# Optimization experiments

Hardware: AMD Instinct MI355X
Metric: run time of the kernel (lower is better)

The kernel has to match this reference:

```python
import jax, jax.numpy as jnp
import numpy as np
from jax import lax

D, H, DK, L, FF, V, B, S = 384, 12, 32, 6, 1536, 30522, 16, 512

def _logit(p):
    return float(np.log(p / (1.0 - p)))

def setup_inputs():
    key = jax.random.key(0)
    ks = jax.random.split(key, 16)
    def g(i, shape, scale=0.02):
        return jax.random.normal(ks[i], shape, jnp.float32) * scale
    return {
        "input_ids": jax.random.randint(ks[0], (B, S), 0, V),
        "attention_mask": jnp.ones((B, S), jnp.int32),
        "emb_tok": g(1, (V, D)),
        "emb_pos": g(2, (S, D)),
        "emb_type": g(3, (2, D)),
        "emb_ln_g": jnp.ones((D,), jnp.float32),
        "emb_ln_b": jnp.zeros((D,), jnp.float32),
        "Wq": g(4, (L, D, D)), "bq": jnp.zeros((L, D), jnp.float32),
        "Wk": g(5, (L, D, D)), "bk": jnp.zeros((L, D), jnp.float32),
        "Wv": g(6, (L, D, D)), "bv": jnp.zeros((L, D), jnp.float32),
        "Wbeta": g(7, (L, D, H)), "bbeta": jnp.zeros((L, H), jnp.float32),
        "decay_fast": jnp.full((L, H), _logit(0.3), jnp.float32),
        "decay_slow": jnp.full((L, H), _logit(0.85), jnp.float32),
        "mix_logit": jnp.zeros((L, H), jnp.float32),
        "Wg": g(8, (L, D, D)),
        "Wo": g(9, (L, D, D)), "bo": jnp.zeros((L, D), jnp.float32),
        "attn_ln_g": jnp.ones((L, D), jnp.float32), "attn_ln_b": jnp.zeros((L, D), jnp.float32),
        "Wffn1": g(10, (L, D, FF)), "bffn1": jnp.zeros((L, FF), jnp.float32),
        "Wffn2": g(11, (L, FF, D)), "bffn2": jnp.zeros((L, D), jnp.float32),
        "ffn_ln_g": jnp.ones((L, D), jnp.float32), "ffn_ln_b": jnp.zeros((L, D), jnp.float32),
    }

def _ln(x, g, b, eps=1e-12):
    m = x.mean(-1, keepdims=True)
    v = ((x - m) ** 2).mean(-1, keepdims=True)
    return (x - m) * lax.rsqrt(v + eps) * g + b

def _delta_attn(x, mask_f, Wq, bq, Wk, bk, Wv, bv, Wbeta, bbeta, df_logit, ds_logit, mix_logit, Wg, Wo, bo):
    # Hierarchical delta-rule linear attention: O(n) recurrence, two decay timescales.
    Bz, Sq, _ = x.shape
    q = jax.nn.silu((x @ Wq + bq).reshape(Bz, Sq, H, DK))
    k = jax.nn.silu((x @ Wk + bk).reshape(Bz, Sq, H, DK))
    k = k / (jnp.linalg.norm(k, axis=-1, keepdims=True) + 1e-6)
    v = (x @ Wv + bv).reshape(Bz, Sq, H, DK)
    beta = jax.nn.sigmoid(x @ Wbeta + bbeta) * mask_f[..., None]  # [B,S,H]
    df = jax.nn.sigmoid(df_logit)[None, :, None, None]  # fast decay, per head
    ds = jax.nn.sigmoid(ds_logit)[None, :, None, None]  # slow decay, per head
    qT = q.transpose(1, 0, 2, 3)  # time-major [S,B,H,DK]
    kT = k.transpose(1, 0, 2, 3)
    vT = v.transpose(1, 0, 2, 3)
    betaT = beta.transpose(1, 0, 2)

    def step(carry, xs):
        Sf, Ss = carry  # [B,H,DK,DK] fast/slow memory states
        kt, vt, qt, bt = xs
        err_f = (vt - jnp.einsum('bhk,bhkv->bhv', kt, Sf)) * bt[..., None]
        Sf = df * Sf + jnp.einsum('bhk,bhv->bhkv', kt, err_f)
        err_s = (vt - jnp.einsum('bhk,bhkv->bhv', kt, Ss)) * bt[..., None]
        Ss = ds * Ss + jnp.einsum('bhk,bhv->bhkv', kt, err_s)
        of = jnp.einsum('bhk,bhkv->bhv', qt, Sf)
        os = jnp.einsum('bhk,bhkv->bhv', qt, Ss)
        return (Sf, Ss), (of, os)

    S0 = jnp.zeros((Bz, H, DK, DK), x.dtype)
    _, (ofT, osT) = lax.scan(step, (S0, S0), (kT, vT, qT, betaT))
    mix = jax.nn.sigmoid(mix_logit)[None, None, :, None]
    o = mix * ofT.transpose(1, 0, 2, 3) + (1.0 - mix) * osT.transpose(1, 0, 2, 3)
    o = o.reshape(Bz, Sq, D)
    o = o * jax.nn.sigmoid(x @ Wg)  # enhanced-flux output gate
    return o @ Wo + bo

def reference(input_ids, attention_mask, emb_tok, emb_pos, emb_type, emb_ln_g, emb_ln_b, Wq, bq, Wk, bk, Wv, bv, Wbeta, bbeta, decay_fast, decay_slow, mix_logit, Wg, Wo, bo, attn_ln_g, attn_ln_b, Wffn1, bffn1, Wffn2, bffn2, ffn_ln_g, ffn_ln_b):
    mask_f = attention_mask.astype(jnp.float32)
    h = emb_tok[input_ids] + emb_pos[None, :input_ids.shape[1]] + emb_type[0][None, None]
    h = _ln(h, emb_ln_g, emb_ln_b)
    for i in range(L):
        attn = _delta_attn(h, mask_f, Wq[i], bq[i], Wk[i], bk[i], Wv[i], bv[i], Wbeta[i], bbeta[i], decay_fast[i], decay_slow[i], mix_logit[i], Wg[i], Wo[i], bo[i])
        h = _ln(h + attn, attn_ln_g[i], attn_ln_b[i])
        ffn = jax.nn.gelu(h @ Wffn1[i] + bffn1[i], approximate=False) @ Wffn2[i] + bffn2[i]
        h = _ln(h + ffn, ffn_ln_g[i], ffn_ln_b[i])
    m = mask_f[..., None]
    emb = (h * m).sum(1) / jnp.clip(m.sum(1), 1e-9)
    return emb / (jnp.linalg.norm(emb, axis=1, keepdims=True) + 1e-12)
```

## Files before the change

kernel.cpp:

```cpp
#include <hip/hip_runtime.h>
#include <hip/hip_bf16.h>

#define NTOK   8192
#define DMODEL 384
#define NHEAD  12
#define DHEAD  32
#define NLAYER 6
#define DFF    1536
#define SEQ    512
#define BATCH  16
#define WTAL   1916928L

typedef __attribute__((ext_vector_type(8))) short short8;
typedef __attribute__((ext_vector_type(4))) float f32x4;

__device__ __forceinline__ float sigmoidf_(float x){ return 1.f/(1.f+expf(-x)); }

__device__ __forceinline__ ushort f2b(float x){
  uint b = __builtin_bit_cast(uint, x);
  uint r = (b + 0x7FFFu + ((b>>16)&1u)) >> 16;
  return (ushort)r;
}
__device__ __forceinline__ uint pk2(float lo, float hi){
  return (uint)f2b(lo) | ((uint)f2b(hi)<<16);
}
__device__ __forceinline__ float4 b2f4(uint2 u){
  float4 f;
  f.x = __builtin_bit_cast(float, u.x<<16);
  f.y = __builtin_bit_cast(float, u.x & 0xffff0000u);
  f.z = __builtin_bit_cast(float, u.y<<16);
  f.w = __builtin_bit_cast(float, u.y & 0xffff0000u);
  return f;
}
__device__ __forceinline__ float red8(float x){
  int t = __builtin_amdgcn_update_dpp(0, __builtin_bit_cast(int,x), 0xB1, 0xF, 0xF, true);
  x += __builtin_bit_cast(float,t);
  t = __builtin_amdgcn_update_dpp(0, __builtin_bit_cast(int,x), 0x4E, 0xF, 0xF, true);
  x += __builtin_bit_cast(float,t);
  t = __builtin_amdgcn_update_dpp(0, __builtin_bit_cast(int,x), 0x141, 0xF, 0xF, true);
  x += __builtin_bit_cast(float,t);
  return x;
}
__device__ __forceinline__ void gload16(const ushort* g, ushort* l){
  __builtin_amdgcn_global_load_lds((const __attribute__((address_space(1))) void*)g,
                                   (__attribute__((address_space(3))) void*)l, 16, 0, 0);
}

__device__ __forceinline__ void beta_from_row(
    int n, int tid, const float y0, const float y1, const float y2,
    const float* __restrict__ Wb, const float* __restrict__ bbv,
    const int* __restrict__ amask, float* __restrict__ Bb,
    float (*bred)[13])
{
  float part[12];
  #pragma unroll
  for (int hh=0;hh<12;hh++) part[hh]=0.f;
  #pragma unroll
  for (int j=0;j<3;j++){
    int d = tid + j*128;
    float yv = (j==0)?y0:(j==1)?y1:y2;
    const float* wrow = Wb + (long)d*12;
    #pragma unroll
    for (int hh=0;hh<12;hh++) part[hh] += yv * wrow[hh];
  }
  #pragma unroll
  for (int hh=0;hh<12;hh++) bred[tid][hh] = part[hh];
  __syncthreads();
  if (tid < 96){
    int hh = tid>>3, i = tid&7;
    float s = 0.f;
    #pragma unroll
    for (int k=0;k<16;k++) s += bred[i + 8*k][hh];
    s += __shfl_xor(s,1); s += __shfl_xor(s,2); s += __shfl_xor(s,4);
    if (i==0) Bb[(long)n*NHEAD+hh] = (float)amask[n] * sigmoidf_(s + bbv[hh]);
  }
}

__global__ __launch_bounds__(128) void embed_ln_kernel(
    const int* __restrict__ ids, const float* __restrict__ tok,
    const float* __restrict__ pos, const float* __restrict__ typ,
    const float* __restrict__ g, const float* __restrict__ bvec,
    float* __restrict__ out, ushort* __restrict__ outb,
    const float* __restrict__ Wb0, const float* __restrict__ bb0,
    const int* __restrict__ amask, float* __restrict__ Bb)
{
  __shared__ float r1[2], r2[2];
  __shared__ float bred[128][13];
  int n = blockIdx.x;
  int t = n & (SEQ-1);
  int id = ids[n];
  int tid = threadIdx.x;
  float v[3]; float s1=0.f, s2=0.f;
  #pragma unroll
  for (int j=0;j<3;j++){
    int d = tid + j*128;
    float x = tok[(long)id*DMODEL + d] + pos[t*DMODEL + d] + typ[d];
    v[j]=x; s1+=x; s2+=x*x;
  }
  #pragma unroll
  for (int m=1;m<64;m<<=1){ s1 += __shfl_xor(s1,m); s2 += __shfl_xor(s2,m); }
  if ((tid&63)==0){ r1[tid>>6]=s1; r2[tid>>6]=s2; }
  __syncthreads();
  s1 = r1[0]+r1[1]; s2 = r2[0]+r2[1];
  float mean = s1*(1.f/DMODEL);
  float var  = s2*(1.f/DMODEL) - mean*mean;
  float inv  = rsqrtf(var + 1e-12f);
  float y[3];
  #pragma unroll
  for (int j=0;j<3;j++){
    int d = tid + j*128;
    y[j] = (v[j]-mean)*inv*g[d] + bvec[d];
    out[(long)n*DMODEL + d] = y[j];
    outb[(long)n*DMODEL + d] = f2b(y[j]);
  }
  __syncthreads();
  beta_from_row(n, tid, y[0], y[1], y[2], Wb0, bb0, amask, Bb, bred);
}

__global__ __launch_bounds__(128) void add_ln_kernel(
    float* __restrict__ h, const float* __restrict__ res,
    const float* __restrict__ g, const float* __restrict__ bvec,
    ushort* __restrict__ hb,
    const float* __restrict__ Wbn, const float* __restrict__ bbn,
    const int* __restrict__ amask, float* __restrict__ Bb)
{
  __shared__ float r1[2], r2[2];
  __shared__ float bred[128][13];
  int n = blockIdx.x;
  int tid = threadIdx.x;
  float v[3]; float s1=0.f, s2=0.f;
  #pragma unroll
  for (int j=0;j<3;j++){
    int d = tid + j*128;
    float x = h[(long)n*DMODEL + d] + res[(long)n*DMODEL + d];
    v[j]=x; s1+=x; s2+=x*x;
  }
  #pragma unroll
  for (int m=1;m<64;m<<=1){ s1 += __shfl_xor(s1,m); s2 += __shfl_xor(s2,m); }
  if ((tid&63)==0){ r1[tid>>6]=s1; r2[tid>>6]=s2; }
  __syncthreads();
  s1 = r1[0]+r1[1]; s2 = r2[0]+r2[1];
  float mean = s1*(1.f/DMODEL);
  float var  = s2*(1.f/DMODEL) - mean*mean;
  float inv  = rsqrtf(var + 1e-12f);
  float y[3];
  #pragma unroll
  for (int j=0;j<3;j++){
    int d = tid + j*128;
    y[j] = (v[j]-mean)*inv*g[d] + bvec[d];
    h[(long)n*DMODEL + d] = y[j];
    hb[(long)n*DMODEL + d] = f2b(y[j]);
  }
  if (Wbn){
    __syncthreads();
    beta_from_row(n, tid, y[0], y[1], y[2], Wbn, bbn, amask, Bb, bred);
  }
}

__global__ __launch_bounds__(256) void tcvt6(
    const float* __restrict__ Wq, const float* __restrict__ Wk,
    const float* __restrict__ Wv, const float* __restrict__ Wg,
    const float* __restrict__ Wo, const float* __restrict__ W1,
    const float* __restrict__ W2, ushort* __restrict__ WTA)
{
  __shared__ float tile[32][33];
  int l = blockIdx.x / 1872;
  int bid = blockIdx.x % 1872;
  const float* Wq_l = Wq + (long)l*DMODEL*DMODEL;
  const float* Wk_l = Wk + (long)l*DMODEL*DMODEL;
  const float* Wv_l = Wv + (long)l*DMODEL*DMODEL;
  const float* Wg_l = Wg + (long)l*DMODEL*DMODEL;
  const float* Wo_l = Wo + (long)l*DMODEL*DMODEL;
  const float* W1_l = W1 + (long)l*DMODEL*DFF;
  const float* W2_l = W2 + (long)l*DFF*DMODEL;
  ushort* WTAl = WTA + (long)l*WTAL;

  const float* src; long dstbase; int rowlen, Nd, tk, tn, row0;
  if (bid < 720){
    int seg = bid/144, t = bid%144;
    tk = t%12; tn = t/12;
    src = (seg==0)?Wq_l:(seg==1)?Wk_l:(seg==2)?Wv_l:(seg==3)?Wg_l:Wo_l;
    Nd = 384; rowlen = 384;
    if (seg<4){ dstbase=0; row0=seg*384; }
    else      { dstbase=589824; row0=0; }
  } else if (bid < 1296){
    int t = bid-720; tk=t%12; tn=t/12;
    src=W1_l; Nd=DFF; dstbase=737280; row0=0; rowlen=384;
  } else {
    int t = bid-1296; tk=t%48; tn=t/48;
    src=W2_l; Nd=384; dstbase=1327104; row0=0; rowlen=DFF;
  }
  int k0=tk*32, n0=tn*32;
  int tt=threadIdx.x;
  int r=tt>>3, c4=(tt&7)<<2;
  const float* sp = src + (long)(k0+r)*Nd + n0 + c4;
  float4 f = *(const float4*)sp;
  tile[r][c4+0]=f.x; tile[r][c4+1]=f.y; tile[r][c4+2]=f.z; tile[r][c4+3]=f.w;
  __syncthreads();
  ushort4 o;
  o.x=f2b(tile[c4+0][r]); o.y=f2b(tile[c4+1][r]);
  o.z=f2b(tile[c4+2][r]); o.w=f2b(tile[c4+3][r]);
  *(ushort4*)(WTAl + dstbase + (long)(row0+n0+r)*rowlen + k0 + c4) = o;
}

__device__ __forceinline__ int2 xcd_swz(){
  int lin = blockIdx.y*64 + blockIdx.x;
  int nb = gridDim.x*gridDim.y;
  int s = (lin & 7)*(nb>>3) + (lin>>3);
  return make_int2(s & 63, s >> 6);
}

template<int ACT, int OUTBF>
__global__ __launch_bounds__(256) void gemm_bf(
    const ushort* __restrict__ Xb, const ushort* __restrict__ WT,
    const float* __restrict__ bias, void* __restrict__ Cv, int Kd, int Nd)
{
  __shared__ ushort A_lds[128*32];
  __shared__ ushort B_lds[128*32];
  int tid = threadIdx.x;
  int2 bxy = xcd_swz();
  int bm = bxy.x*128, bn = bxy.y*128;
  int w = tid>>6, lane = tid&63;
  int wm = w>>1, wn = w&1;
  f32x4 acc[4][4];
  #pragma unroll
  for (int i=0;i<4;i++)
    #pragma unroll
    for (int j=0;j<4;j++) acc[i][j]=(f32x4)(0.f);

  int cl = lane&15, koff = (lane>>4)*8;
  int srow = w*32 + (lane>>2);
  int scol = (lane&3)*8;
  const ushort* gA0 = Xb + (long)(bm+srow)*Kd + scol;
  const ushort* gA1 = gA0 + 16*(long)Kd;
  const ushort* gB0 = WT + (long)(bn+srow)*Kd + scol;
  const ushort* gB1 = gB0 + 16*(long)Kd;
  ushort* lA = A_lds + w*1024;
  ushort* lB = B_lds + w*1024;

  for (int k0=0; k0<Kd; k0+=32){
    gload16(gA0+k0, lA);
    gload16(gA1+k0, lA+512);
    gload16(gB0+k0, lB);
    gload16(gB1+k0, lB+512);
    __syncthreads();
    short8 bf[4];
    #pragma unroll
    for (int ni=0;ni<4;ni++)
      bf[ni] = *(const short8*)&B_lds[(wn*64+ni*16+cl)*32 + koff];
    #pragma unroll
    for (int mi=0;mi<4;mi++){
      short8 af = *(const short8*)&A_lds[(wm*64+mi*16+cl)*32 + koff];
      #pragma unroll
      for (int ni=0;ni<4;ni++)
        acc[mi][ni] = __builtin_amdgcn_mfma_f32_16x16x32_bf16(af, bf[ni], acc[mi][ni], 0,0,0);
    }
    __syncthreads();
  }

  int rb = (lane>>4)*4;
  #pragma unroll
  for (int ni=0; ni<4; ni++){
    int col = bn + wn*64 + ni*16 + cl;
    float bsv = bias ? bias[col] : 0.f;
    #pragma unroll
    for (int mi=0; mi<4; mi++){
      #pragma unroll
      for (int j=0;j<4;j++){
        int row = bm + wm*64 + mi*16 + rb + j;
        float c = acc[mi][ni][j] + bsv;
        if (ACT==1)      c = c*sigmoidf_(c);
        else if (ACT==2) c = 0.5f*c*(1.f+erff(c*0.70710678118f));
        else if (ACT==3) c = sigmoidf_(c);
        if (OUTBF) ((ushort*)Cv)[(long)row*Nd + col] = f2b(c);
        else       ((float*)Cv)[(long)row*Nd + col] = c;
      }
    }
  }
}

template<int ACT, int OUTBF>
__global__ __launch_bounds__(256) void gemm_bf2(
    const ushort* __restrict__ Xb, const ushort* __restrict__ WT,
    const float* __restrict__ bias, void* __restrict__ Cv, int Kd, int Nd)
{
  __shared__ ushort A_lds[128*32];
  __shared__ ushort B_lds[64*32];
  int tid = threadIdx.x;
  int2 bxy = xcd_swz();
  int bm = bxy.x*128, bn = bxy.y*64;
  int w = tid>>6, lane = tid&63;
  int wm = w>>1, wn = w&1;
  f32x4 acc[4][2];
  #pragma unroll
  for (int i=0;i<4;i++){ acc[i][0]=(f32x4)(0.f); acc[i][1]=(f32x4)(0.f); }

  int cl = lane&15, koff = (lane>>4)*8;
  int srowA = w*32 + (lane>>2);
  int scol = (lane&3)*8;
  const ushort* gA0 = Xb + (long)(bm+srowA)*Kd + scol;
  const ushort* gA1 = gA0 + 16*(long)Kd;
  int srowB = w*16 + (lane>>2);
  const ushort* gB = WT + (long)(bn+srowB)*Kd + scol;
  ushort* lA = A_lds + w*1024;
  ushort* lB = B_lds + w*512;

  for (int k0=0; k0<Kd; k0+=32){
    gload16(gA0+k0, lA);
    gload16(gA1+k0, lA+512);
    gload16(gB+k0, lB);
    __syncthreads();
    short8 b0 = *(const short8*)&B_lds[(wn*32+cl)*32 + koff];
    short8 b1 = *(const short8*)&B_lds[(wn*32+16+cl)*32 + koff];
    #pragma unroll
    for (int mi=0;mi<4;mi++){
      short8 af = *(const short8*)&A_lds[(wm*64+mi*16+cl)*32 + koff];
      acc[mi][0] = __builtin_amdgcn_mfma_f32_16x16x32_bf16(af, b0, acc[mi][0], 0,0,0);
      acc[mi][1] = __builtin_amdgcn_mfma_f32_16x16x32_bf16(af, b1, acc[mi][1], 0,0,0);
    }
    __syncthreads();
  }

  int rb = (lane>>4)*4;
  #pragma unroll
  for (int ni=0; ni<2; ni++){
    int col = bn + wn*32 + ni*16 + cl;
    float bsv = bias ? bias[col] : 0.f;
    #pragma unroll
    for (int mi=0; mi<4; mi++){
      #pragma unroll
      for (int j=0;j<4;j++){
        int row = bm + wm*64 + mi*16 + rb + j;
        float c = acc[mi][ni][j] + bsv;
        if (ACT==1)      c = c*sigmoidf_(c);
        else if (ACT==2) c = 0.5f*c*(1.f+erff(c*0.70710678118f));
        else if (ACT==3) c = sigmoidf_(c);
        if (OUTBF) ((ushort*)Cv)[(long)row*Nd + col] = f2b(c);
        else       ((float*)Cv)[(long)row*Nd + col] = c;
      }
    }
  }
}

__global__ __launch_bounds__(256) void gemm_qkvg(
    const ushort* __restrict__ Xb, const ushort* __restrict__ WT,
    const float* __restrict__ bq, const float* __restrict__ bk,
    const float* __restrict__ bv, ushort* __restrict__ C)
{
  __shared__ ushort A_lds[128*32];
  __shared__ ushort B_lds[128*32];
  int tid = threadIdx.x;
  int2 bxy = xcd_swz();
  int bm = bxy.x*128, bn = bxy.y*128;
  int w = tid>>6, lane = tid&63;
  int wm = w>>1, wn = w&1;
  f32x4 acc[4][4];
  #pragma unroll
  for (int i=0;i<4;i++)
    #pragma unroll
    for (int j=0;j<4;j++) acc[i][j]=(f32x4)(0.f);

  int cl = lane&15, koff = (lane>>4)*8;
  int srow = w*32 + (lane>>2);
  int scol = (lane&3)*8;
  const ushort* gA0 = Xb + (long)(bm+srow)*DMODEL + scol;
  const ushort* gA1 = gA0 + 16*DMODEL;
  const ushort* gB0 = WT + (long)(bn+srow)*DMODEL + scol;
  const ushort* gB1 = gB0 + 16*DMODEL;
  ushort* lA = A_lds + w*1024;
  ushort* lB = B_lds + w*1024;

  for (int k0=0; k0<DMODEL; k0+=32){
    gload16(gA0+k0, lA);
    gload16(gA1+k0, lA+512);
    gload16(gB0+k0, lB);
    gload16(gB1+k0, lB+512);
    __syncthreads();
    short8 bf[4];
    #pragma unroll
    for (int ni=0;ni<4;ni++)
      bf[ni] = *(const short8*)&B_lds[(wn*64+ni*16+cl)*32 + koff];
    #pragma unroll
    for (int mi=0;mi<4;mi++){
      short8 af = *(const short8*)&A_lds[(wm*64+mi*16+cl)*32 + koff];
      #pragma unroll
      for (int ni=0;ni<4;ni++)
        acc[mi][ni] = __builtin_amdgcn_mfma_f32_16x16x32_bf16(af, bf[ni], acc[mi][ni], 0,0,0);
    }
    __syncthreads();
  }

  int seg = bxy.y/3;
  const float* bp = (seg==0)?bq:(seg==1)?bk:(seg==2)?bv:nullptr;
  int boff = seg*384;
  int rb = (lane>>4)*4;
  #pragma unroll
  for (int ni=0; ni<4; ni++){
    int col = bn + wn*64 + ni*16 + cl;
    float bsv = bp ? bp[col-boff] : 0.f;
    #pragma unroll
    for (int mi=0; mi<4; mi++){
      #pragma unroll
      for (int j=0;j<4;j++){
        int row = bm + wm*64 + mi*16 + rb + j;
        float c = acc[mi][ni][j] + bsv;
        if (seg<2)       c = c*sigmoidf_(c);
        else if (seg==3) c = sigmoidf_(c);
        C[(long)row*DFF + col] = f2b(c);
      }
    }
  }
}

__global__ __launch_bounds__(512,2) void scan12_kernel(
    const ushort* __restrict__ QKVGb, const float* __restrict__ Bb,
    const float* __restrict__ dfl, const float* __restrict__ dsl,
    const float* __restrict__ mixl, ushort* __restrict__ OA)
{
  __shared__ float Qc[66][36], Kc[66][36], Vt[32][68], Bc[68], Ofs[2][64][36];
  int bh = blockIdx.x;
  int b = bh / NHEAD, hh = bh - b*NHEAD;
  int tid = threadIdx.x;
  int w = tid>>6, lane = tid&63;
  int st = w>>2, vq = w&3;
  int kq = lane&7, v = vq*8 + (lane>>3);
  float dec = sigmoidf_(st ? dsl[hh] : dfl[hh]);
  float mix = sigmoidf_(mixl[hh]);
  long rowbase = (long)b*SEQ;
  const ushort* rp = QKVGb + rowbase*DFF + hh*32;
  const float* bp = Bb + rowbase*NHEAD + hh;

  int r0 = tid>>3, c40 = (tid&7)<<2;
  float S[4] = {0.f,0.f,0.f,0.f};

  float4 sq, sk, sv; float sb = 0.f;
  {
    long g = (long)r0*DFF;
    sq = b2f4(*(const uint2*)(rp + g + c40));
    sk = b2f4(*(const uint2*)(rp + g + 384 + c40));
    sv = b2f4(*(const uint2*)(rp + g + 768 + c40));
    if (tid < 64) sb = bp[(long)tid*NHEAD];
    float ss = red8(sk.x*sk.x + sk.y*sk.y + sk.z*sk.z + sk.w*sk.w);
    float inv = 1.f/(sqrtf(ss)+1e-6f);
    sk.x*=inv; sk.y*=inv; sk.z*=inv; sk.w*=inv;
    *(float4*)&Qc[r0][c40] = sq;
    *(float4*)&Kc[r0][c40] = sk;
    Vt[c40+0][r0]=sv.x; Vt[c40+1][r0]=sv.y; Vt[c40+2][r0]=sv.z; Vt[c40+3][r0]=sv.w;
    if (tid < 64) Bc[tid] = sb;
  }
  __syncthreads();

  for (int c=0; c<8; ++c){
    if (c < 7){
      long g = (long)((c+1)*64 + r0)*DFF;
      sq = b2f4(*(const uint2*)(rp + g + c40));
      sk = b2f4(*(const uint2*)(rp + g + 384 + c40));
      sv = b2f4(*(const uint2*)(rp + g + 768 + c40));
      if (tid < 64) sb = bp[(long)((c+1)*64 + tid)*NHEAD];
    }
    float4 g4 = b2f4(*(const uint2*)(rp + (long)(c*64 + r0)*DFF + 1152 + c40));
    __builtin_amdgcn_sched_barrier(0);

    float4 kA = *(const float4*)&Kc[0][kq*4];
    float4 qA = *(const float4*)&Qc[0][kq*4];
    float4 kB = *(const float4*)&Kc[1][kq*4];
    float4 qB = *(const float4*)&Qc[1][kq*4];
    float vrA[4], brA[4], vrB[4], brB[4];
    *(float4*)vrA = *(const float4*)&Vt[v][0];
    *(float4*)brA = *(const float4*)&Bc[0];

    for (int t8=0; t8<8; ++t8){
      *(float4*)vrB = *(const float4*)&Vt[v][(2*t8+1)*4];
      *(float4*)brB = *(const float4*)&Bc[(2*t8+1)*4];
      #pragma unroll
      for (int i=0;i<4;i++){
        int t = t8*8 + i;
        float4 kN = *(const float4*)&Kc[t+2][kq*4];
        float4 qN = *(const float4*)&Qc[t+2][kq*4];
        float pa = kA.x*S[0] + kA.y*S[1];
        float pb = kA.z*S[2] + kA.w*S[3];
        float p = red8(pa+pb);
        float err = (vrA[i] - p)*brA[i];
        S[0] = dec*S[0] + kA.x*err;
        S[1] = dec*S[1] + kA.y*err;
        S[2] = dec*S[2] + kA.z*err;
        S[3] = dec*S[3] + kA.w*err;
        float oa = qA.x*S[0] + qA.y*S[1];
        float ob = qA.z*S[2] + qA.w*S[3];
        float o = red8(oa+ob);
        if (kq==0) Ofs[st][t][v] = o;
        kA=kB; qA=qB; kB=kN; qB=qN;
      }
      *(float4*)vrA = *(const float4*)&Vt[v][(2*t8+2)*4];
      *(float4*)brA = *(const float4*)&Bc[(2*t8+2)*4];
      #pragma unroll
      for (int i=0;i<4;i++){
        int t = t8*8 + 4 + i;
        float4 kN = *(const float4*)&Kc[t+2][kq*4];
        float4 qN = *(const float4*)&Qc[t+2][kq*4];
        float pa = kA.x*S[0] + kA.y*S[1];
        float pb = kA.z*S[2] + kA.w*S[3];
        float p = red8(pa+pb);
        float err = (vrB[i] - p)*brB[i];
        S[0] = dec*S[0] + kA.x*err;
        S[1] = dec*S[1] + kA.y*err;
        S[2] = dec*S[2] + kA.z*err;
        S[3] = dec*S[3] + kA.w*err;
        float oa = qA.x*S[0] + qA.y*S[1];
        float ob = qA.z*S[2] + qA.w*S[3];
        float o = red8(oa+ob);
        if (kq==0) Ofs[st][t][v] = o;
        kA=kB; qA=qB; kB=kN; qB=qN;
      }
    }
    __syncthreads();

    {
      float4 of = *(const float4*)&Ofs[0][r0][c40];
      float4 os = *(const float4*)&Ofs[1][r0][c40];
      float a0 = (mix*of.x + (1.f-mix)*os.x)*g4.x;
      float a1 = (mix*of.y + (1.f-mix)*os.y)*g4.y;
      float a2 = (mix*of.z + (1.f-mix)*os.z)*g4.z;
      float a3 = (mix*of.w + (1.f-mix)*os.w)*g4.w;
      uint2 o2; o2.x = pk2(a0,a1); o2.y = pk2(a2,a3);
      *(uint2*)(OA + (rowbase + c*64 + r0)*DMODEL + hh*32 + c40) = o2;
    }
    if (c < 7){
      *(float4*)&Qc[r0][c40] = sq;
      *(float4*)&Kc[r0][c40] = sk;
      Vt[c40+0][r0]=sv.x; Vt[c40+1][r0]=sv.y; Vt[c40+2][r0]=sv.z; Vt[c40+3][r0]=sv.w;
      if (tid < 64) Bc[tid] = sb;
    }
    __syncthreads();
  }
}

__global__ __launch_bounds__(384) void pool_norm_kernel(
    const float* __restrict__ h, const int* __restrict__ mask, float* __restrict__ out)
{
  int b = blockIdx.x; int d = threadIdx.x;
  float s=0.f, ms=0.f;
  for (int t=0;t<SEQ;t++){
    float m = (float)mask[b*SEQ+t];
    s += h[((long)b*SEQ+t)*DMODEL + d]*m;
    ms += m;
  }
  float emb = s / fmaxf(ms, 1e-9f);
  float ss = emb*emb;
  #pragma unroll
  for (int m2=1;m2<64;m2<<=1) ss += __shfl_xor(ss,m2);
  __shared__ float r[6];
  if ((d&63)==0) r[d>>6]=ss;
  __syncthreads();
  ss = r[0]+r[1]+r[2]+r[3]+r[4]+r[5];
  out[b*DMODEL+d] = emb / (sqrtf(ss)+1e-12f);
}

extern "C" void kernel_launch(void* const* d_in, const int* in_sizes, int n_in,
                              void* d_out, int out_size, void* d_ws, size_t ws_size,
                              hipStream_t stream)
{
  const int*   ids   = (const int*)d_in[0];
  const int*   amask = (const int*)d_in[1];
  const float* etok  = (const float*)d_in[2];
  const float* epos  = (const float*)d_in[3];
  const float* etyp  = (const float*)d_in[4];
  const float* elng  = (const float*)d_in[5];
  const float* elnb  = (const float*)d_in[6];
  const float* Wq = (const float*)d_in[7];  const float* bq = (const float*)d_in[8];
  const float* Wk = (const float*)d_in[9];  const float* bk = (const float*)d_in[10];
  const float* Wv = (const float*)d_in[11]; const float* bv = (const float*)d_in[12];
  const float* Wb = (const float*)d_in[13]; const float* bb = (const float*)d_in[14];
  const float* dfl = (const float*)d_in[15];
  const float* dsl = (const float*)d_in[16];
  const float* mixl= (const float*)d_in[17];
  const float* Wg = (const float*)d_in[18];
  const float* Wo = (const float*)d_in[19]; const float* bo = (const float*)d_in[20];
  const float* alng = (const float*)d_in[21]; const float* alnb = (const float*)d_in[22];
  const float* W1 = (const float*)d_in[23]; const float* b1 = (const float*)d_in[24];
  const float* W2 = (const float*)d_in[25]; const float* b2 = (const float*)d_in[26];
  const float* flng = (const float*)d_in[27]; const float* flnb = (const float*)d_in[28];

  float* ws = (float*)d_ws;
  const long TD = (long)NTOK*DMODEL;
  float* h      = ws;
  ushort* hbf   = (ushort*)(h + TD);
  ushort* QKVGb = (ushort*)(h + TD + TD/2);
  ushort* OA    = (ushort*)(h + TD + TD/2 + 2*TD);
  float* Rb     = h + TD + TD/2 + 2*TD + TD/2;
  float* Bb     = Rb + TD;
  ushort* WTA   = (ushort*)(Bb + (long)NTOK*NHEAD);
  ushort* F1B   = QKVGb;

  embed_ln_kernel<<<NTOK,128,0,stream>>>(ids, etok, epos, etyp, elng, elnb, h, hbf,
                                         Wb, bb, amask, Bb);
  tcvt6<<<6*1872,256,0,stream>>>(Wq, Wk, Wv, Wg, Wo, W1, W2, WTA);

  for (int l=0;l<NLAYER;l++){
    ushort* WTAl = WTA + (long)l*WTAL;
    gemm_qkvg<<<dim3(64,12),256,0,stream>>>(hbf, WTAl, bq+l*DMODEL, bk+l*DMODEL, bv+l*DMODEL, QKVGb);
    scan12_kernel<<<BATCH*NHEAD,512,0,stream>>>(QKVGb, Bb, dfl + l*NHEAD, dsl + l*NHEAD, mixl + l*NHEAD, OA);
    gemm_bf2<0,0><<<dim3(64,6),256,0,stream>>>(OA, WTAl+589824, bo + l*DMODEL, Rb, DMODEL, DMODEL);
    add_ln_kernel<<<NTOK,128,0,stream>>>(h, Rb, alng + (long)l*DMODEL, alnb + (long)l*DMODEL, hbf,
                                         nullptr, nullptr, amask, Bb);
    gemm_bf<2,1><<<dim3(64,12),256,0,stream>>>(hbf, WTAl+737280, b1 + (long)l*DFF, F1B, DMODEL, DFF);
    gemm_bf2<0,0><<<dim3(64,6),256,0,stream>>>(F1B, WTAl+1327104, b2 + (long)l*DMODEL, Rb, DFF, DMODEL);
    const float* Wbn = (l+1<NLAYER) ? (Wb + (long)(l+1)*DMODEL*NHEAD) : nullptr;
    const float* bbn = (l+1<NLAYER) ? (bb + (long)(l+1)*NHEAD) : nullptr;
    add_ln_kernel<<<NTOK,128,0,stream>>>(h, Rb, flng + (long)l*DMODEL, flnb + (long)l*DMODEL, hbf,
                                         Wbn, bbn, amask, Bb);
  }

  pool_norm_kernel<<<BATCH,384,0,stream>>>(h, amask, (float*)d_out);
}
```

Before: 1.146 ms.

## Double-buffer LDS tiles in bf16 GEMM kernels to overlap loads with MFMA

Converts the three MFMA GEMM kernels from single-buffered LDS staging, with two barriers per K step, to ping-pong A/B buffers. The next K tile's global-to-LDS load is issued before the current tile's MFMAs, with a single waitcnt and barrier per step. This hides global load latency behind compute and halves barrier count. LDS use doubles per block, which may lower occupancy. The loop also assumes an even number of K iterations.

```diff
diff --git a/kernel.cpp b/kernel.cpp
--- a/kernel.cpp
+++ b/kernel.cpp
@@ -215,8 +215,7 @@
     const ushort* __restrict__ Xb, const ushort* __restrict__ WT,
     const float* __restrict__ bias, void* __restrict__ Cv, int Kd, int Nd)
 {
-  __shared__ ushort A_lds[128*32];
-  __shared__ ushort B_lds[128*32];
+  __shared__ ushort A0[128*32], A1[128*32], B0[128*32], B1[128*32];
   int tid = threadIdx.x;
   int2 bxy = xcd_swz();
   int bm = bxy.x*128, bn = bxy.y*128;
@@ -231,31 +230,57 @@
   int cl = lane&15, koff = (lane>>4)*8;
   int srow = w*32 + (lane>>2);
   int scol = (lane&3)*8;
-  const ushort* gA0 = Xb + (long)(bm+srow)*Kd + scol;
-  const ushort* gA1 = gA0 + 16*(long)Kd;
-  const ushort* gB0 = WT + (long)(bn+srow)*Kd + scol;
-  const ushort* gB1 = gB0 + 16*(long)Kd;
-  ushort* lA = A_lds + w*1024;
-  ushort* lB = B_lds + w*1024;
-
-  for (int k0=0; k0<Kd; k0+=32){
-    gload16(gA0+k0, lA);
-    gload16(gA1+k0, lA+512);
-    gload16(gB0+k0, lB);
-    gload16(gB1+k0, lB+512);
-    __syncthreads();
-    short8 bf[4];
-    #pragma unroll
-    for (int ni=0;ni<4;ni++)
-      bf[ni] = *(const short8*)&B_lds[(wn*64+ni*16+cl)*32 + koff];
-    #pragma unroll
-    for (int mi=0;mi<4;mi++){
-      short8 af = *(const short8*)&A_lds[(wm*64+mi*16+cl)*32 + koff];
-      #pragma unroll
-      for (int ni=0;ni<4;ni++)
-        acc[mi][ni] = __builtin_amdgcn_mfma_f32_16x16x32_bf16(af, bf[ni], acc[mi][ni], 0,0,0);
-    }
-    __syncthreads();
+  const ushort* gA0p = Xb + (long)(bm+srow)*Kd + scol;
+  const ushort* gA1p = gA0p + 16*(long)Kd;
+  const ushort* gB0p = WT + (long)(bn+srow)*Kd + scol;
+  const ushort* gB1p = gB0p + 16*(long)Kd;
+  int lofA = w*1024, lofB = w*1024;
+  int NI = Kd >> 5;
+
+  gload16(gA0p, A0+lofA); gload16(gA1p, A0+lofA+512);
+  gload16(gB0p, B0+lofB); gload16(gB1p, B0+lofB+512);
+  asm volatile("s_waitcnt vmcnt(0)" ::: "memory");
+  __builtin_amdgcn_s_barrier();
+
+  for (int it=0; it<NI; it+=2){
+    {
+      short8 bfr[4], afr[4];
+      #pragma unroll
+      for (int ni=0;ni<4;ni++) bfr[ni] = *(const short8*)&B0[(wn*64+ni*16+cl)*32 + koff];
+      #pragma unroll
+      for (int mi=0;mi<4;mi++) afr[mi] = *(const short8*)&A0[(wm*64+mi*16+cl)*32 + koff];
+      int k0 = (it+1)<<5;
+      gload16(gA0p+k0, A1+lofA); gload16(gA1p+k0, A1+lofA+512);
+      gload16(gB0p+k0, B1+lofB); gload16(gB1p+k0, B1+lofB+512);
+      #pragma unroll
+      for (int mi=0;mi<4;mi++)
+        #pragma unroll
+        for (int ni=0;ni<4;ni++)
+          acc[mi][ni] = __builtin_amdgcn_mfma_f32_16x16x32_bf16(afr[mi], bfr[ni], acc[mi][ni], 0,0,0);
+      asm volatile("s_waitcnt vmcnt(0)" ::: "memory");
+      __builtin_amdgcn_s_barrier();
+    }
+    {
+      short8 bfr[4], afr[4];
+      #pragma unroll
+      for (int ni=0;ni<4;ni++) bfr[ni] = *(const short8*)&B1[(wn*64+ni*16+cl)*32 + koff];
+      #pragma unroll
+      for (int mi=0;mi<4;mi++) afr[mi] = *(const short8*)&A1[(wm*64+mi*16+cl)*32 + koff];
+      if (it+2 < NI){
+        int k0 = (it+2)<<5;
+        gload16(gA0p+k0, A0+lofA); gload16(gA1p+k0, A0+lofA+512);
+        gload16(gB0p+k0, B0+lofB); gload16(gB1p+k0, B0+lofB+512);
+      }
+      #pragma unroll
+      for (int mi=0;mi<4;mi++)
+        #pragma unroll
+        for (int ni=0;ni<4;ni++)
+          acc[mi][ni] = __builtin_amdgcn_mfma_f32_16x16x32_bf16(afr[mi], bfr[ni], acc[mi][ni], 0,0,0);
+      if (it+2 < NI){
+        asm volatile("s_waitcnt vmcnt(0)" ::: "memory");
+        __builtin_amdgcn_s_barrier();
+      }
+    }
   }
 
   int rb = (lane>>4)*4;
@@ -284,8 +309,7 @@
     const ushort* __restrict__ Xb, const ushort* __restrict__ WT,
     const float* __restrict__ bias, void* __restrict__ Cv, int Kd, int Nd)
 {
-  __shared__ ushort A_lds[128*32];
-  __shared__ ushort B_lds[64*32];
+  __shared__ ushort A0[128*32], A1[128*32], B0[64*32], B1[64*32];
   int tid = threadIdx.x;
   int2 bxy = xcd_swz();
   int bm = bxy.x*128, bn = bxy.y*64;
@@ -298,27 +322,54 @@
   int cl = lane&15, koff = (lane>>4)*8;
   int srowA = w*32 + (lane>>2);
   int scol = (lane&3)*8;
-  const ushort* gA0 = Xb + (long)(bm+srowA)*Kd + scol;
-  const ushort* gA1 = gA0 + 16*(long)Kd;
+  const ushort* gA0p = Xb + (long)(bm+srowA)*Kd + scol;
+  const ushort* gA1p = gA0p + 16*(long)Kd;
   int srowB = w*16 + (lane>>2);
-  const ushort* gB = WT + (long)(bn+srowB)*Kd + scol;
-  ushort* lA = A_lds + w*1024;
-  ushort* lB = B_lds + w*512;
-
-  for (int k0=0; k0<Kd; k0+=32){
-    gload16(gA0+k0, lA);
-    gload16(gA1+k0, lA+512);
-    gload16(gB+k0, lB);
-    __syncthreads();
-    short8 b0 = *(const short8*)&B_lds[(wn*32+cl)*32 + koff];
-    short8 b1 = *(const short8*)&B_lds[(wn*32+16+cl)*32 + koff];
-    #pragma unroll
-    for (int mi=0;mi<4;mi++){
-      short8 af = *(const short8*)&A_lds[(wm*64+mi*16+cl)*32 + koff];
-      acc[mi][0] = __builtin_amdgcn_mfma_f32_16x16x32_bf16(af, b0, acc[mi][0], 0,0,0);
-      acc[mi][1] = __builtin_amdgcn_mfma_f32_16x16x32_bf16(af, b1, acc[mi][1], 0,0,0);
-    }
-    __syncthreads();
+  const ushort* gBp = WT + (long)(bn+srowB)*Kd + scol;
+  int lofA = w*1024, lofB = w*512;
+  int NI = Kd >> 5;
+
+  gload16(gA0p, A0+lofA); gload16(gA1p, A0+lofA+512); gload16(gBp, B0+lofB);
+  asm volatile("s_waitcnt vmcnt(0)" ::: "memory");
+  __builtin_amdgcn_s_barrier();
+
+  for (int it=0; it<NI; it+=2){
+    {
+      short8 b0r = *(const short8*)&B0[(wn*32+cl)*32 + koff];
+      short8 b1r = *(const short8*)&B0[(wn*32+16+cl)*32 + koff];
+      short8 afr[4];
+      #pragma unroll
+      for (int mi=0;mi<4;mi++) afr[mi] = *(const short8*)&A0[(wm*64+mi*16+cl)*32 + koff];
+      int k0 = (it+1)<<5;
+      gload16(gA0p+k0, A1+lofA); gload16(gA1p+k0, A1+lofA+512); gload16(gBp+k0, B1+lofB);
+      #pragma unroll
+      for (int mi=0;mi<4;mi++){
+        acc[mi][0] = __builtin_amdgcn_mfma_f32_16x16x32_bf16(afr[mi], b0r, acc[mi][0], 0,0,0);
+        acc[mi][1] = __builtin_amdgcn_mfma_f32_16x16x32_bf16(afr[mi], b1r, acc[mi][1], 0,0,0);
+      }
+      asm volatile("s_waitcnt vmcnt(0)" ::: "memory");
+      __builtin_amdgcn_s_barrier();
+    }
+    {
+      short8 b0r = *(const short8*)&B1[(wn*32+cl)*32 + koff];
+      short8 b1r = *(const short8*)&B1[(wn*32+16+cl)*32 + koff];
+      short8 afr[4];
+      #pragma unroll
+      for (int mi=0;mi<4;mi++) afr[mi] = *(const short8*)&A1[(wm*64+mi*16+cl)*32 + koff];
+      if (it+2 < NI){
+        int k0 = (it+2)<<5;
+        gload16(gA0p+k0, A0+lofA); gload16(gA1p+k0, A0+lofA+512); gload16(gBp+k0, B0+lofB);
+      }
+      #pragma unroll
+      for (int mi=0;mi<4;mi++){
+        acc[mi][0] = __builtin_amdgcn_mfma_f32_16x16x32_bf16(afr[mi], b0r, acc[mi][0], 0,0,0);
+        acc[mi][1] = __builtin_amdgcn_mfma_f32_16x16x32_bf16(afr[mi], b1r, acc[mi][1], 0,0,0);
+      }
+      if (it+2 < NI){
+        asm volatile("s_waitcnt vmcnt(0)" ::: "memory");
+        __builtin_amdgcn_s_barrier();
+      }
+    }
   }
 
   int rb = (lane>>4)*4;
@@ -347,8 +398,7 @@
     const float* __restrict__ bq, const float* __restrict__ bk,
     const float* __restrict__ bv, ushort* __restrict__ C)
 {
-  __shared__ ushort A_lds[128*32];
-  __shared__ ushort B_lds[128*32];
+  __shared__ ushort A0[128*32], A1[128*32], B0[128*32], B1[128*32];
   int tid = threadIdx.x;
   int2 bxy = xcd_swz();
   int bm = bxy.x*128, bn = bxy.y*128;
@@ -363,31 +413,57 @@
   int cl = lane&15, koff = (lane>>4)*8;
   int srow = w*32 + (lane>>2);
   int scol = (lane&3)*8;
-  const ushort* gA0 = Xb + (long)(bm+srow)*DMODEL + scol;
-  const ushort* gA1 = gA0 + 16*DMODEL;
-  const ushort* gB0 = WT + (long)(bn+srow)*DMODEL + scol;
-  const ushort* gB1 = gB0 + 16*DMODEL;
-  ushort* lA = A_lds + w*1024;
-  ushort* lB = B_lds + w*1024;
-
-  for (int k0=0; k0<DMODEL; k0+=32){
-    gload16(gA0+k0, lA);
-    gload16(gA1+k0, lA+512);
-    gload16(gB0+k0, lB);
-    gload16(gB1+k0, lB+512);
-    __syncthreads();
-    short8 bf[4];
-    #pragma unroll
-    for (int ni=0;ni<4;ni++)
-      bf[ni] = *(const short8*)&B_lds[(wn*64+ni*16+cl)*32 + koff];
-    #pragma unroll
-    for (int mi=0;mi<4;mi++){
-      short8 af = *(const short8*)&A_lds[(wm*64+mi*16+cl)*32 + koff];
-      #pragma unroll
-      for (int ni=0;ni<4;ni++)
-        acc[mi][ni] = __builtin_amdgcn_mfma_f32_16x16x32_bf16(af, bf[ni], acc[mi][ni], 0,0,0);
-    }
-    __syncthreads();
+  const ushort* gA0p = Xb + (long)(bm+srow)*DMODEL + scol;
+  const ushort* gA1p = gA0p + 16*DMODEL;
+  const ushort* gB0p = WT + (long)(bn+srow)*DMODEL + scol;
+  const ushort* gB1p = gB0p + 16*DMODEL;
+  int lofA = w*1024, lofB = w*1024;
+  const int NI = DMODEL >> 5;
+
+  gload16(gA0p, A0+lofA); gload16(gA1p, A0+lofA+512);
+  gload16(gB0p, B0+lofB); gload16(gB1p, B0+lofB+512);
+  asm volatile("s_waitcnt vmcnt(0)" ::: "memory");
+  __builtin_amdgcn_s_barrier();
+
+  for (int it=0; it<NI; it+=2){
+    {
+      short8 bfr[4], afr[4];
+      #pragma unroll
+      for (int ni=0;ni<4;ni++) bfr[ni] = *(const short8*)&B0[(wn*64+ni*16+cl)*32 + koff];
+      #pragma unroll
+      for (int mi=0;mi<4;mi++) afr[mi] = *(const short8*)&A0[(wm*64+mi*16+cl)*32 + koff];
+      int k0 = (it+1)<<5;
+      gload16(gA0p+k0, A1+lofA); gload16(gA1p+k0, A1+lofA+512);
+      gload16(gB0p+k0, B1+lofB); gload16(gB1p+k0, B1+lofB+512);
+      #pragma unroll
+      for (int mi=0;mi<4;mi++)
+        #pragma unroll
+        for (int ni=0;ni<4;ni++)
+          acc[mi][ni] = __builtin_amdgcn_mfma_f32_16x16x32_bf16(afr[mi], bfr[ni], acc[mi][ni], 0,0,0);
+      asm volatile("s_waitcnt vmcnt(0)" ::: "memory");
+      __builtin_amdgcn_s_barrier();
+    }
+    {
+      short8 bfr[4], afr[4];
+      #pragma unroll
+      for (int ni=0;ni<4;ni++) bfr[ni] = *(const short8*)&B1[(wn*64+ni*16+cl)*32 + koff];
+      #pragma unroll
+      for (int mi=0;mi<4;mi++) afr[mi] = *(const short8*)&A1[(wm*64+mi*16+cl)*32 + koff];
+      if (it+2 < NI){
+        int k0 = (it+2)<<5;
+        gload16(gA0p+k0, A0+lofA); gload16(gA1p+k0, A0+lofA+512);
+        gload16(gB0p+k0, B0+lofB); gload16(gB1p+k0, B0+lofB+512);
+      }
+      #pragma unroll
+      for (int mi=0;mi<4;mi++)
+        #pragma unroll
+        for (int ni=0;ni<4;ni++)
+          acc[mi][ni] = __builtin_amdgcn_mfma_f32_16x16x32_bf16(afr[mi], bfr[ni], acc[mi][ni], 0,0,0);
+      if (it+2 < NI){
+        asm volatile("s_waitcnt vmcnt(0)" ::: "memory");
+        __builtin_amdgcn_s_barrier();
+      }
+    }
   }
 
   int seg = bxy.y/3;
```

New measurement: 1.185 ms. +3.4%, slower.
